# Kernel optimization log

Measured on AMD Instinct MI355X. Metric: run time of the kernel, lower is better.

Reference implementation:

```python
import jax, jax.numpy as jnp
import numpy as np

VOCAB_SIZE = 32000
PAD_IDX = 0


def setup_inputs() -> dict:
    key = jax.random.key(0)
    k1, k2 = jax.random.split(key)
    tokens = jax.random.randint(k1, (256, 2048), 0, VOCAB_SIZE, dtype=jnp.int64 if jax.config.jax_enable_x64 else jnp.int32)
    lengths = jax.random.randint(k2, (256,), 0, 2048, dtype=tokens.dtype)
    return {"tokens": tokens, "lengths": lengths}


def reference(tokens, lengths):
    # Faithful to torch OneHotEncoder.forward:
    #   onehot[b,t,:] = one_hot(tokens[b,t]) with pad_idx column zeroed per position,
    #   then summed over t -> counts [batch, vocab]. NOTE: the torch code computes a
    #   clamped `outhot` but RETURNS the un-clamped `onehot` counts; we match that.
    # Efficient form: direct per-row scatter-add histogram, skipping pad tokens,
    # without materializing the [B, T, V] intermediate.
    B, T = tokens.shape
    rows = jnp.arange(B)[:, None]  # [B,1] broadcasts against tokens [B,T]
    contrib = jnp.where(tokens == PAD_IDX, 0.0, 1.0).astype(jnp.float32)
    counts = jnp.zeros((B, VOCAB_SIZE), dtype=jnp.float32).at[rows, tokens].add(contrib)
    # pad_idx column is always zeroed (scatter of 0 at pad_selector per position)
    counts = counts.at[:, PAD_IDX].set(0.0)
    return counts
```

## Files before the change

kernel.cpp:

```cpp
#include <hip/hip_runtime.h>


#define VOCAB  32000
#define CHUNKS 4
#define CV     (VOCAB / CHUNKS)
#define BLOCK  256

typedef float f32x4 __attribute__((ext_vector_type(4)));

__global__ __launch_bounds__(BLOCK)
void OneHotEncoder_43052752175267_kernel(const int* __restrict__ tokens,
                                         float* __restrict__ out,
                                         int T) {
    __shared__ __align__(16) unsigned int hist[CV / 2];

    const int row   = blockIdx.x >> 2;
    const int chunk = blockIdx.x & (CHUNKS - 1);
    const int lo    = chunk * CV;
    const int tid   = threadIdx.x;

    uint4* h4 = (uint4*)hist;
    const uint4 z = make_uint4(0u, 0u, 0u, 0u);
    for (int i = tid; i < CV / 8; i += BLOCK)
        h4[i] = z;
    __syncthreads();

    const int* trow = tokens + (long long)row * T;
    for (int i = tid; i < T; i += BLOCK) {
        int tok = trow[i];
        unsigned local = (unsigned)(tok - lo);
        if (tok != 0 && local < (unsigned)CV)
            atomicAdd(&hist[local >> 1], 1u << ((local & 1) << 4));
    }
    __syncthreads();

    f32x4* o4 = (f32x4*)(out + (long long)row * VOCAB + lo);
    const uint2* h2 = (const uint2*)hist;
    for (int i = tid; i < CV / 4; i += BLOCK) {
        uint2 h = h2[i];
        f32x4 f;
        f.x = (float)(h.x & 0xFFFFu);
        f.y = (float)(h.x >> 16);
        f.z = (float)(h.y & 0xFFFFu);
        f.w = (float)(h.y >> 16);
        __builtin_nontemporal_store(f, &o4[i]);
    }
}

extern "C" void kernel_launch(void* const* d_in, const int* in_sizes, int n_in,
                              void* d_out, int out_size, void* d_ws, size_t ws_size,
                              hipStream_t stream) {
    const int* tokens = (const int*)d_in[0];
    const int B = in_sizes[1];
    const int T = in_sizes[0] / B;
    float* out = (float*)d_out;

    OneHotEncoder_43052752175267_kernel<<<dim3(B * CHUNKS), dim3(BLOCK), 0, stream>>>(tokens, out, T);
}
```

Before: 69.05 us.

## Split vocab into 8 chunks, vectorize token loads, reorder block mapping, drop nontemporal stores

Raises the vocab chunk count from 4 to 8, which halves shared histogram size and doubles the number of blocks. Blocks are now mapped chunk-major so neighbouring blocks read different token rows. Tokens are loaded as int4 with a scalar tail loop, and the output uses ordinary stores instead of nontemporal ones. More chunks means each token row is read from global memory twice as many times, and plain stores may change cache behaviour for the large output write.

```diff
diff --git a/kernel.cpp b/kernel.cpp
--- a/kernel.cpp
+++ b/kernel.cpp
@@ -2,20 +2,18 @@
 
 
 #define VOCAB  32000
-#define CHUNKS 4
+#define CHUNKS 8
 #define CV     (VOCAB / CHUNKS)
 #define BLOCK  256
-
-typedef float f32x4 __attribute__((ext_vector_type(4)));
 
 __global__ __launch_bounds__(BLOCK)
 void OneHotEncoder_43052752175267_kernel(const int* __restrict__ tokens,
                                          float* __restrict__ out,
-                                         int T) {
+                                         int T, int B) {
     __shared__ __align__(16) unsigned int hist[CV / 2];
 
-    const int row   = blockIdx.x >> 2;
-    const int chunk = blockIdx.x & (CHUNKS - 1);
+    const int row   = blockIdx.x % B;
+    const int chunk = blockIdx.x / B;
     const int lo    = chunk * CV;
     const int tid   = threadIdx.x;
 
@@ -26,7 +24,20 @@
     __syncthreads();
 
     const int* trow = tokens + (long long)row * T;
-    for (int i = tid; i < T; i += BLOCK) {
+    const int nt4 = T >> 2;
+    const int4* t4 = (const int4*)trow;
+    for (int i = tid; i < nt4; i += BLOCK) {
+        int4 t = t4[i];
+        unsigned l0 = (unsigned)(t.x - lo);
+        unsigned l1 = (unsigned)(t.y - lo);
+        unsigned l2 = (unsigned)(t.z - lo);
+        unsigned l3 = (unsigned)(t.w - lo);
+        if (t.x != 0 && l0 < (unsigned)CV) atomicAdd(&hist[l0 >> 1], 1u << ((l0 & 1) << 4));
+        if (t.y != 0 && l1 < (unsigned)CV) atomicAdd(&hist[l1 >> 1], 1u << ((l1 & 1) << 4));
+        if (t.z != 0 && l2 < (unsigned)CV) atomicAdd(&hist[l2 >> 1], 1u << ((l2 & 1) << 4));
+        if (t.w != 0 && l3 < (unsigned)CV) atomicAdd(&hist[l3 >> 1], 1u << ((l3 & 1) << 4));
+    }
+    for (int i = (nt4 << 2) + tid; i < T; i += BLOCK) {
         int tok = trow[i];
         unsigned local = (unsigned)(tok - lo);
         if (tok != 0 && local < (unsigned)CV)
@@ -34,16 +45,16 @@
     }
     __syncthreads();
 
-    f32x4* o4 = (f32x4*)(out + (long long)row * VOCAB + lo);
+    float4* o4 = (float4*)(out + (long long)row * VOCAB + lo);
     const uint2* h2 = (const uint2*)hist;
     for (int i = tid; i < CV / 4; i += BLOCK) {
         uint2 h = h2[i];
-        f32x4 f;
+        float4 f;
         f.x = (float)(h.x & 0xFFFFu);
         f.y = (float)(h.x >> 16);
         f.z = (float)(h.y & 0xFFFFu);
         f.w = (float)(h.y >> 16);
-        __builtin_nontemporal_store(f, &o4[i]);
+        o4[i] = f;
     }
 }
 
@@ -55,5 +66,6 @@
     const int T = in_sizes[0] / B;
     float* out = (float*)d_out;
 
-    OneHotEncoder_43052752175267_kernel<<<dim3(B * CHUNKS), dim3(BLOCK), 0, stream>>>(tokens, out, T);
+    OneHotEncoder_43052752175267_kernel<<<dim3(B * CHUNKS), dim3(BLOCK), 0, stream>>>(
+        tokens, out, T, B);
 }
```

After: 66.27 us. -4.0%, faster.
